# Kernel tuning notes

Measured on AMD Instinct MI355X. Metric: run time of the kernel, lower is better.

## Reference

```python
import jax, jax.numpy as jnp
import numpy as np

B = 32          # graphs per batch
NPG = 512       # nodes per graph
EPG = 2048      # original edges per graph (stored in y[:, -1])
N = B * NPG     # 16384 nodes
E = B * EPG     # 65536 edges
GF = 5          # num_global_features
ETOT = E + N    # edges after add_self_loops

def _lin(k, o, i):
    return jax.random.normal(k, (o, i), jnp.float32) / np.sqrt(i)

def setup_inputs():
    key = jax.random.key(0)
    ks = jax.random.split(key, 20)
    x = jax.random.normal(ks[0], (N,), jnp.float32)
    off = (jnp.arange(B, dtype=jnp.int32) * NPG)[:, None]
    src = (jax.random.randint(ks[1], (B, EPG), 0, NPG, dtype=jnp.int32) + off).reshape(-1)
    dst = (jax.random.randint(ks[2], (B, EPG), 0, NPG, dtype=jnp.int32) + off).reshape(-1)
    edge_index = jnp.stack([src, dst])
    edge_attr = jax.random.normal(ks[3], (E, GF), jnp.float32)
    # last global feature = number of edges per graph (module reads y[:, -1])
    y = jax.random.normal(ks[4], (B, GF), jnp.float32).at[:, -1].set(float(EPG)).reshape(-1)
    batch_vector = jnp.repeat(jnp.arange(B, dtype=jnp.int32), NPG)
    p = dict(
        Wn=_lin(ks[5], 512, 1), bn=jnp.zeros(512, jnp.float32),
        We=_lin(ks[6], 511, GF), be=jnp.zeros(511, jnp.float32),
        Wg=_lin(ks[7], 512, GF), bg=jnp.zeros(512, jnp.float32),
        Wl=_lin(ks[8], 1024, 512), bl=jnp.zeros(1024, jnp.float32),
        Wr=_lin(ks[9], 1024, 512), br=jnp.zeros(1024, jnp.float32),
        Wge=_lin(ks[10], 1024, 511),
        att=jax.random.normal(ks[11], (1024,), jnp.float32) / 32.0,
        bgat=jnp.zeros(1024, jnp.float32),
        Wm=_lin(ks[12], 1024, 1024), bm=jnp.zeros(1024, jnp.float32),
        Wmi=_lin(ks[13], 1024, 1024), bmi=jnp.zeros(1024, jnp.float32),
        Wce=_lin(ks[14], 1024, 512), bce=jnp.zeros(1024, jnp.float32),
        W1=_lin(ks[15], 256, 2048), b1=jnp.zeros(256, jnp.float32),
        W2=_lin(ks[16], 1, 256), b2=jnp.zeros(1, jnp.float32),
    )
    return dict(x=x, edge_index=edge_index, edge_attr=edge_attr, y=y,
                batch_vector=batch_vector, **p)

def _leaky(v, s=0.01):
    return jnp.where(v >= 0, v, s * v)

def _forward(edge_index, batch_vector, x, edge_attr, y, Wn, bn, We, be, Wg, bg,
             Wl, bl, Wr, br, Wge, att, bgat, Wm, bm, Wmi, bmi, Wce, bce,
             W1, b1, W2, b2):
    # add_self_loops (fill_value=1.0 for edge_attr), self loops appended last
    loops = jnp.arange(N, dtype=edge_index.dtype)
    src = jnp.concatenate([edge_index[0], loops])
    dst = jnp.concatenate([edge_index[1], loops])
    ea = jnp.concatenate([edge_attr, jnp.ones((N, GF), edge_attr.dtype)], axis=0)
    # preprocessing MLPs (dropout = identity at inference)
    h = _leaky(x[:, None] @ Wn.T + bn)               # [N, 512]
    e = _leaky(ea @ We.T + be)                       # [ETOT, 511]
    yg = _leaky(y.reshape(B, GF) @ Wg.T + bg)        # [B, 512]
    # GATv2Conv, 1 head, concat, negative_slope=0.2, no self-loop add
    xl = h @ Wl.T + bl                               # source transform [N, 1024]
    xr = h @ Wr.T + br                               # target transform [N, 1024]
    m = _leaky(xl[src] + xr[dst] + e @ Wge.T, 0.2)   # [ETOT, 1024]
    logit = m @ att                                  # [ETOT]
    mx = jax.ops.segment_max(logit, dst, num_segments=N)
    ex = jnp.exp(logit - mx[dst])
    alpha = ex / (jax.ops.segment_sum(ex, dst, num_segments=N)[dst] + 1e-16)
    gat = jax.ops.segment_sum(alpha[:, None] * xl[src], dst, num_segments=N) + bgat
    edge_total = jnp.concatenate([e, alpha[:, None]], axis=1)  # [ETOT, 512]
    # GeneralConv: undirected message, add aggregation, identity skip (in==out)
    hm = gat @ Wm.T + bm
    hmi = gat @ Wmi.T + bmi
    eh = edge_total @ Wce.T + bce                    # [ETOT, 1024]
    deg = jax.ops.segment_sum(jnp.ones((ETOT,), gat.dtype), dst, num_segments=N)
    conv = (jax.ops.segment_sum(hm[src] + eh, dst, num_segments=N)
            + deg[:, None] * hmi + gat)              # [N, 1024]
    # global mean pooling (nodes) and module's contiguous edge batch vector
    nc = jax.ops.segment_sum(jnp.ones((N,), conv.dtype), batch_vector, num_segments=B)
    pn = jax.ops.segment_sum(conv, batch_vector, num_segments=B) / nc[:, None]
    ebatch = jnp.repeat(jnp.arange(B, dtype=jnp.int32), EPG + NPG)
    pe = jax.ops.segment_sum(edge_total, ebatch, num_segments=B) / float(EPG + NPG)
    pooled = jnp.concatenate([pn, pe, yg], axis=1)   # [B, 2048]
    out = _leaky(pooled @ W1.T + b1) @ W2.T + b2
    return jax.nn.sigmoid(out)                       # [B, 1]

def reference(x, edge_index, edge_attr, y, batch_vector, Wn, bn, We, be, Wg, bg,
              Wl, bl, Wr, br, Wge, att, bgat, Wm, bm, Wmi, bmi, Wce, bce,
              W1, b1, W2, b2):
    return _forward(edge_index, batch_vector, x, edge_attr, y, Wn, bn, We, be,
                    Wg, bg, Wl, bl, Wr, br, Wge, att, bgat, Wm, bm, Wmi, bmi,
                    Wce, bce, W1, b1, W2, b2)
```

## Files before the change

kernel.cpp:

```cpp
#include <hip/hip_runtime.h>
#include <cstdint>
#include <cstddef>

#define N_NODES 16384
#define N_EDGES 65536
#define ETOT    81920
#define B_GR    32

typedef __attribute__((ext_vector_type(8))) short bf16x8;
typedef __attribute__((ext_vector_type(4))) float f32x4;

static constexpr size_t OFF_XL    = 0;
static constexpr size_t OFF_XR    = 33554432ULL;
static constexpr size_t OFF_EBF   = 67108864ULL;
static constexpr size_t OFF_SORT  = 67108864ULL;
static constexpr size_t OFF_TAB   = 67125248ULL;
static constexpr size_t TABSZ     = 513ULL*2048ULL*4ULL;
static constexpr size_t OFF_WT    = OFF_TAB + 4*TABSZ;
static constexpr size_t OFF_SEG   = OFF_WT + 4194304ULL;
static constexpr size_t SEGSZ     = 32ULL*2048ULL*4ULL;
static constexpr size_t OFF_ALPHA = 67502336ULL;
static constexpr size_t OFF_ADJ   = 67830016ULL;
static constexpr size_t OFF_WGEP  = 134217728ULL;
static constexpr size_t OFF_LPART = 135266304ULL;
static constexpr size_t OFF_DEG   = 137363456ULL;
static constexpr size_t OFF_ODEG  = 137428992ULL;
static constexpr size_t OFF_CURS  = 137494528ULL;
static constexpr size_t OFF_PG    = 137560064ULL;
static constexpr size_t OFF_PDG   = 137691136ULL;
static constexpr size_t OFF_PGAT  = 137822208ULL;
static constexpr size_t OFF_PS    = 137953280ULL;
static constexpr size_t OFF_PE    = 138018816ULL;
static constexpr size_t OFF_WLOOP = 138084352ULL;
static constexpr size_t OFF_YG    = 138088448ULL;
static constexpr size_t OFF_PN    = 138153984ULL;
static constexpr size_t OFF_OPRE  = 138285056ULL;

__device__ __forceinline__ float leaky01(float v){ return v >= 0.f ? v : 0.01f*v; }
__device__ __forceinline__ float leaky02(float v){ return v >= 0.f ? v : 0.2f*v; }
__device__ __forceinline__ unsigned short f2bf(float f){
  union { float f; unsigned u; } v; v.f = f;
  unsigned r = v.u + 0x7FFFu + ((v.u >> 16) & 1u);
  return (unsigned short)(r >> 16);
}
__device__ __forceinline__ float bf2f(unsigned short h){
  union { unsigned u; float f; } v; v.u = ((unsigned)h) << 16;
  return v.f;
}

__global__ __launch_bounds__(256) void k_prep0(
    const float* __restrict__ Wge, const float* __restrict__ y,
    const float* __restrict__ Wg, const float* __restrict__ bg,
    const float* __restrict__ We, const float* __restrict__ be,
    const float* __restrict__ Wn, const float* __restrict__ bn,
    const float* __restrict__ Wl, const float* __restrict__ Wr,
    float* __restrict__ zone, unsigned short* __restrict__ Wge_p,
    float* __restrict__ yg, float* __restrict__ we_loop,
    float* __restrict__ WT,
    float* __restrict__ sTpos, float* __restrict__ sTneg,
    int* __restrict__ posIdx, int* __restrict__ negIdx, int* __restrict__ meta) {
  __shared__ union {
    float e_lds[512];
    float tile[64][65];
    struct { float tS[512]; int gS[512]; int zflag; } srt;
  } shm;
  int bx = blockIdx.x, tid = threadIdx.x;
  if (bx < 176) {
    ((float4*)zone)[bx*256 + tid] = (float4){0.f,0.f,0.f,0.f};
  } else if (bx < 2224) {
    int gid = (bx-176)*256 + tid;
    int j = gid >> 9, k = gid & 511;
    Wge_p[gid] = (k < 511) ? f2bf(Wge[(size_t)j*511 + k]) : (unsigned short)0;
  } else if (bx < 2288) {
    int gid = (bx-2224)*256 + tid;
    int b = gid >> 9, j = gid & 511;
    float s = bg[j];
    #pragma unroll
    for (int k=0;k<5;k++) s += y[b*5+k]*Wg[j*5+k];
    yg[gid] = leaky01(s);
  } else if (bx < 2292) {
    for (int c = tid; c < 512; c += 256) {
      float v = 0.f;
      if (c < 511) {
        float s = be[c];
        #pragma unroll
        for (int q=0;q<5;q++) s += We[c*5+q];
        v = leaky01(s);
      }
      shm.e_lds[c] = v;
    }
    __syncthreads();
    int j = (bx-2288)*256 + tid;
    float s = 0.f;
    for (int k=0;k<511;k++) s += shm.e_lds[k]*Wge[(size_t)j*511+k];
    we_loop[j] = s;
  } else if (bx < 2548) {
    int t = bx - 2292;
    int jt = t & 31, kt = t >> 5;
    #pragma unroll
    for (int i=0;i<16;i++){
      int idx = tid + i*256;
      int jj = idx >> 6, kk = idx & 63;
      int j = jt*64 + jj, k = kt*64 + kk;
      float v = (j < 1024) ? Wl[(size_t)j*512 + k] : Wr[(size_t)(j-1024)*512 + k];
      shm.tile[kk][jj] = v;
    }
    __syncthreads();
    #pragma unroll
    for (int i=0;i<16;i++){
      int idx = tid + i*256;
      int kk = idx >> 6, jj = idx & 63;
      WT[(size_t)(kt*64 + kk)*2048 + jt*64 + jj] = shm.tile[kk][jj];
    }
  } else {
    const float INF = __builtin_inff();
    if (tid == 0) shm.srt.zflag = 0;
    __syncthreads();
    for (int kk = tid; kk < 512; kk += 256) {
      float wn = Wn[kk], bk = bn[kk];
      int gp; float t;
      if (wn > 0.f)      { gp = 1; t = -bk/wn; }
      else if (wn < 0.f) { gp = 0; t = -bk/wn; }
      else               { gp = 1; t = (bk >= 0.f) ? -INF : INF; }
      shm.srt.tS[kk] = t; shm.srt.gS[kk] = gp;
      if (bk != 0.f) atomicOr(&shm.srt.zflag, 1);
    }
    __syncthreads();
    int cp = 0;
    for (int m = 0; m < 512; m++) cp += shm.srt.gS[m];
    int cn = 512 - cp;
    for (int kk = tid; kk < 512; kk += 256) {
      float t = shm.srt.tS[kk]; int gp = shm.srt.gS[kk];
      int rank = 0;
      for (int m = 0; m < 512; m++) {
        if (shm.srt.gS[m] == gp) {
          float tm = shm.srt.tS[m];
          bool lt = gp ? (tm < t) : (tm > t);
          if (lt || (tm == t && m < kk)) rank++;
        }
      }
      if (gp) { sTpos[rank] = t; posIdx[rank] = kk; }
      else    { sTneg[rank] = t; negIdx[rank] = kk; }
      if (kk >= cp) { sTpos[kk] = INF;  posIdx[kk] = 0; }
      if (kk >= cn) { sTneg[kk] = -INF; negIdx[kk] = 0; }
    }
    if (tid == 0) { meta[0] = cp; meta[1] = cn; meta[2] = (shm.srt.zflag == 0) ? 1 : 0; }
  }
}


__global__ __launch_bounds__(256) void k_tab_sum(
    const float* __restrict__ WT,
    const float* __restrict__ Wn, const float* __restrict__ bn,
    const int* __restrict__ posIdx, const int* __restrict__ negIdx,
    const int* __restrict__ meta,
    float* __restrict__ segAP, float* __restrict__ segAN,
    float* __restrict__ segBP, float* __restrict__ segBN) {
  __shared__ float wnS[512], bnS[512];
  __shared__ int piS[512], niS[512];
  int tid = threadIdx.x;
  for (int i = tid; i < 512; i += 256) {
    wnS[i] = Wn[i]; bnS[i] = bn[i]; piS[i] = posIdx[i]; niS[i] = negIdx[i];
  }
  __syncthreads();
  int seg = blockIdx.x >> 3, jb = blockIdx.x & 7;
  int j = jb*256 + tid;
  int cntP = meta[0], cntN = meta[1], bz = meta[2];
  float aP=0.f, aN=0.f, bP=0.f, bN=0.f;
  for (int i = 0; i < 16; i++) {
    int r = seg*16 + i;
    if (r < cntP) { int k = piS[r]; float w = WT[(size_t)k*2048 + j]; aP += w*wnS[k]; if (!bz) bP += w*bnS[k]; }
    if (r < cntN) { int k = niS[r]; float w = WT[(size_t)k*2048 + j]; aN += w*wnS[k]; if (!bz) bN += w*bnS[k]; }
  }
  segAP[seg*2048 + j] = aP; segAN[seg*2048 + j] = aN;
  if (!bz) { segBP[seg*2048 + j] = bP; segBN[seg*2048 + j] = bN; }
}

__global__ __launch_bounds__(256) void k_tab_write(
    const float* __restrict__ WT,
    const float* __restrict__ Wn, const float* __restrict__ bn,
    const int* __restrict__ posIdx, const int* __restrict__ negIdx,
    const int* __restrict__ meta,
    const float* __restrict__ segAP, const float* __restrict__ segAN,
    const float* __restrict__ segBP, const float* __restrict__ segBN,
    float* __restrict__ SAp, float* __restrict__ SAn,
    float* __restrict__ SBp, float* __restrict__ SBn) {
  __shared__ float wnS[512], bnS[512];
  __shared__ int piS[512], niS[512];
  int tid = threadIdx.x;
  for (int i = tid; i < 512; i += 256) {
    wnS[i] = Wn[i]; bnS[i] = bn[i]; piS[i] = posIdx[i]; niS[i] = negIdx[i];
  }
  __syncthreads();
  int seg = blockIdx.x >> 3, jb = blockIdx.x & 7;
  int j = jb*256 + tid;
  int cntP = meta[0], cntN = meta[1], bz = meta[2];
  float oAP=0.f, oAN=0.f, oBP=0.f, oBN=0.f;
  for (int s = 0; s < seg; s++) {
    oAP += segAP[s*2048 + j]; oAN += segAN[s*2048 + j];
    if (!bz) { oBP += segBP[s*2048 + j]; oBN += segBN[s*2048 + j]; }
  }
  if (seg == 0) {
    SAp[j] = 0.f; SAn[j] = 0.f;
    if (!bz) { SBp[j] = 0.f; SBn[j] = 0.f; }
  }
  for (int i = 0; i < 16; i++) {
    int r = seg*16 + i;
    if (r < cntP) { int k = piS[r]; float w = WT[(size_t)k*2048 + j]; oAP += w*wnS[k]; if (!bz) oBP += w*bnS[k]; }
    if (r < cntN) { int k = niS[r]; float w = WT[(size_t)k*2048 + j]; oAN += w*wnS[k]; if (!bz) oBN += w*bnS[k]; }
    size_t o = (size_t)(r+1)*2048 + j;
    SAp[o] = oAP; SAn[o] = oAN;
    if (!bz) { SBp[o] = oBP; SBn[o] = oBN; }
  }
}

__global__ __launch_bounds__(256) void k_xlxr(
    const float* __restrict__ x,
    const float* __restrict__ sTpos, const float* __restrict__ sTneg,
    const int* __restrict__ meta,
    const float* __restrict__ SAp, const float* __restrict__ SAn,
    const float* __restrict__ SBp, const float* __restrict__ SBn,
    const float* __restrict__ bl, const float* __restrict__ br,
    unsigned short* __restrict__ xl_bf, unsigned short* __restrict__ xr_bf) {
  __shared__ float totA[2048], totB[2048];
  __shared__ float xS[8];
  __shared__ int rpS[8], rnS[8];
  int tid = threadIdx.x, bid = blockIdx.x;
  int cntP = meta[0], cntN = meta[1], bnzero = meta[2];
  for (int i = tid; i < 2048; i += 256) {
    totA[i] = 0.01f*(SAp[(size_t)cntP*2048 + i] + SAn[(size_t)cntN*2048 + i]);
    totB[i] = bnzero ? 0.f : 0.01f*(SBp[(size_t)cntP*2048 + i] + SBn[(size_t)cntN*2048 + i]);
  }
  if (tid < 8) {
    int n = bid*8 + tid;
    float xv = x[n];
    xS[tid] = xv;
    int lo = 0, hi = 512;
    while (lo < hi) { int mid = (lo+hi)>>1; if (sTpos[mid] <= xv) lo = mid+1; else hi = mid; }
    rpS[tid] = lo;
    lo = 0; hi = 512;
    while (lo < hi) { int mid = (lo+hi)>>1; if (sTneg[mid] >= xv) lo = mid+1; else hi = mid; }
    rnS[tid] = lo;
  }
  __syncthreads();
  int j0 = tid*8;
  bool isL = (j0 < 1024);
  const float* bias = isL ? (bl + j0) : (br + (j0 - 1024));
  float4 bb0 = *(const float4*)(bias);
  float4 bb1 = *(const float4*)(bias + 4);
  float bv[8] = {bb0.x,bb0.y,bb0.z,bb0.w,bb1.x,bb1.y,bb1.z,bb1.w};
  unsigned short* O = isL ? xl_bf : xr_bf;
  int jc = j0 & 1023;
  for (int i = 0; i < 8; i++) {
    int n = bid*8 + i;
    float xv = xS[i];
    size_t rp = (size_t)rpS[i]*2048 + j0, rn = (size_t)rnS[i]*2048 + j0;
    float4 a0 = *(const float4*)(SAp + rp); float4 a1 = *(const float4*)(SAp + rp + 4);
    float4 c0 = *(const float4*)(SAn + rn); float4 c1 = *(const float4*)(SAn + rn + 4);
    float pa[8] = {a0.x+c0.x, a0.y+c0.y, a0.z+c0.z, a0.w+c0.w,
                   a1.x+c1.x, a1.y+c1.y, a1.z+c1.z, a1.w+c1.w};
    float pb[8] = {0.f,0.f,0.f,0.f,0.f,0.f,0.f,0.f};
    if (!bnzero) {
      float4 d0 = *(const float4*)(SBp + rp); float4 d1 = *(const float4*)(SBp + rp + 4);
      float4 e0 = *(const float4*)(SBn + rn); float4 e1 = *(const float4*)(SBn + rn + 4);
      pb[0]=d0.x+e0.x; pb[1]=d0.y+e0.y; pb[2]=d0.z+e0.z; pb[3]=d0.w+e0.w;
      pb[4]=d1.x+e1.x; pb[5]=d1.y+e1.y; pb[6]=d1.z+e1.z; pb[7]=d1.w+e1.w;
    }
    unsigned short o[8];
    #pragma unroll
    for (int q=0;q<8;q++) {
      float cA = totA[j0+q] + 0.99f*pa[q];
      float cB = totB[j0+q] + 0.99f*pb[q];
      o[q] = f2bf(xv*cA + cB + bv[q]);
    }
    *(uint4*)(O + (size_t)n*1024 + jc) = *(const uint4*)o;
  }
}

__global__ __launch_bounds__(256) void k_prep_e(
    const float* __restrict__ ea, const float* __restrict__ We, const float* __restrict__ be,
    unsigned short* __restrict__ E_bf,
    const int* __restrict__ ei, int* __restrict__ deg, int* __restrict__ odeg) {
  int blk = blockIdx.x;
  if (blk < 16384) {
    int gid = blk*256 + threadIdx.x;
    int e = gid >> 6, cg = gid & 63;
    int c0 = cg*8;
    const float* e5 = ea + (size_t)e*5;
    float a0=e5[0], a1=e5[1], a2=e5[2], a3=e5[3], a4=e5[4];
    unsigned short o[8];
    #pragma unroll
    for (int j=0;j<8;j++) {
      int c = c0 + j;
      float v = 0.f;
      if (c < 511) {
        const float* w = We + c*5;
        float s = be[c] + a0*w[0] + a1*w[1] + a2*w[2] + a3*w[3] + a4*w[4];
        v = leaky01(s);
      }
      o[j] = f2bf(v);
    }
    ((uint4*)E_bf)[gid] = *(const uint4*)o;
  } else {
    int i = (blk-16384)*256 + threadIdx.x;
    int s, d;
    if (i < N_EDGES) { s = ei[i]; d = ei[N_EDGES + i]; }
    else { s = i - N_EDGES; d = s; }
    atomicAdd(&deg[d], 1);
    atomicAdd(&odeg[s], 1);
  }
}

__global__ void k_fill_adj(const int* __restrict__ ei, int* __restrict__ cursor,
                           int* __restrict__ adj) {
  int i = blockIdx.x*blockDim.x + threadIdx.x;
  int d = (i < N_EDGES) ? ei[N_EDGES + i] : (i - N_EDGES);
  int pos = atomicAdd(&cursor[d], 1);
  if (pos < 64) adj[(size_t)d*64 + pos] = i;
}


__global__ __launch_bounds__(256) void k_mfma_we(
    const unsigned short* __restrict__ E_bf, const unsigned short* __restrict__ Wge_bf,
    const int* __restrict__ ei,
    const unsigned short* __restrict__ xl_bf, const unsigned short* __restrict__ xr_bf,
    const float* __restrict__ att, float* __restrict__ logit_part) {
  __shared__ unsigned short As[2][4096];
  __shared__ unsigned short Bs[2][4096];
  __shared__ float tmp[128];
  int blk = blockIdx.x;
  int xcd = blk & 7, slot = blk >> 3;
  int bx = xcd*64 + (slot >> 3), by = slot & 7;
  int row0 = bx*128, col0 = by*128;
  int tid = threadIdx.x;
  int w = tid >> 6, lane = tid & 63;
  int wm = w >> 1, wn = w & 1;
  int quad = lane >> 4, l16 = lane & 15;
  int ldoff = w*512 + lane*8;
  const unsigned short* gA = E_bf  + (size_t)(row0 + w*16 + l16)*512 + quad*8;
  const unsigned short* gB = Wge_bf + (size_t)(col0 + w*16 + l16)*512 + quad*8;
  f32x4 acc[4][4];
  #pragma unroll
  for (int i=0;i<4;i++)
    #pragma unroll
    for (int j=0;j<4;j++) acc[i][j] = (f32x4){0.f,0.f,0.f,0.f};

  {
    uint4 a0 = *(const uint4*)(gA);
    uint4 a1 = *(const uint4*)(gA + 32768);
    uint4 b0 = *(const uint4*)(gB);
    uint4 b1 = *(const uint4*)(gB + 32768);
    *(uint4*)&As[0][ldoff] = a0; *(uint4*)&As[0][2048+ldoff] = a1;
    *(uint4*)&Bs[0][ldoff] = b0; *(uint4*)&Bs[0][2048+ldoff] = b1;
  }
  __syncthreads();
  int cur = 0;
  #pragma unroll 2
  for (int k0 = 32; k0 <= 512; k0 += 32) {
    uint4 na0, na1, nb0, nb1;
    bool more = (k0 < 512);
    if (more) {
      na0 = *(const uint4*)(gA + k0);
      na1 = *(const uint4*)(gA + 32768 + k0);
      nb0 = *(const uint4*)(gB + k0);
      nb1 = *(const uint4*)(gB + 32768 + k0);
    }
    bf16x8 af[4], bfr[4];
    #pragma unroll
    for (int mi=0;mi<4;mi++)
      af[mi] = *(const bf16x8*)&As[cur][(wm*4+mi)*512 + quad*128 + l16*8];
    #pragma unroll
    for (int ni=0;ni<4;ni++)
      bfr[ni] = *(const bf16x8*)&Bs[cur][(wn*4+ni)*512 + quad*128 + l16*8];
    #pragma unroll
    for (int mi=0;mi<4;mi++)
      #pragma unroll
      for (int ni=0;ni<4;ni++)
        acc[mi][ni] = __builtin_amdgcn_mfma_f32_16x16x32_bf16(af[mi], bfr[ni], acc[mi][ni], 0, 0, 0);
    if (more) {
      *(uint4*)&As[cur^1][ldoff] = na0; *(uint4*)&As[cur^1][2048+ldoff] = na1;
      *(uint4*)&Bs[cur^1][ldoff] = nb0; *(uint4*)&Bs[cur^1][2048+ldoff] = nb1;
    }
    __syncthreads();
    cur ^= 1;
  }
  float att4[4];
  #pragma unroll
  for (int ni=0;ni<4;ni++) att4[ni] = att[col0 + wn*64 + ni*16 + l16];
  float pv[4][4];
  #pragma unroll
  for (int mi=0;mi<4;mi++) {
    #pragma unroll
    for (int r=0;r<4;r++) {
      int e = row0 + wm*64 + mi*16 + quad*4 + r;
      int s = ei[e], d = ei[N_EDGES + e];
      const unsigned short* xlr = xl_bf + (size_t)s*1024;
      const unsigned short* xrr = xr_bf + (size_t)d*1024;
      float p = 0.f;
      #pragma unroll
      for (int ni=0;ni<4;ni++) {
        int col = col0 + wn*64 + ni*16 + l16;
        float z = acc[mi][ni][r] + bf2f(xlr[col]) + bf2f(xrr[col]);
        z = leaky02(z);
        p += z*att4[ni];
      }
      p += __shfl_down(p, 8, 16);
      p += __shfl_down(p, 4, 16);
      p += __shfl_down(p, 2, 16);
      p += __shfl_down(p, 1, 16);
      pv[mi][r] = p;
    }
  }
  if (wn == 1 && l16 == 0) {
    #pragma unroll
    for (int mi=0;mi<4;mi++)
      #pragma unroll
      for (int r=0;r<4;r++)
        tmp[wm*64 + mi*16 + quad*4 + r] = pv[mi][r];
  }
  __syncthreads();
  if (wn == 0 && l16 == 0) {
    #pragma unroll
    for (int mi=0;mi<4;mi++)
      #pragma unroll
      for (int r=0;r<4;r++) {
        int le = wm*64 + mi*16 + quad*4 + r;
        logit_part[(size_t)(row0 + le)*8 + by] = pv[mi][r] + tmp[le];
      }
  }
}

__global__ __launch_bounds__(256) void k_softmax_gat(
    const int* __restrict__ ei, const int* __restrict__ deg, const int* __restrict__ adj,
    const float* __restrict__ logit_part,
    const unsigned short* __restrict__ xl_bf, const unsigned short* __restrict__ xr_bf,
    const float* __restrict__ we_loop, const float* __restrict__ att,
    const float* __restrict__ bgat,
    float* __restrict__ alpha, unsigned short* __restrict__ gat_bf) {
  int blk = blockIdx.x;
  int wid = threadIdx.x >> 6, lane = threadIdx.x & 63;
  int n = ((blk & 7) << 11) + ((blk >> 3) << 2) + wid;
  int c0 = lane*16;

  float sll;
  {
    const uint4* xp = (const uint4*)(xl_bf + (size_t)n*1024 + c0);
    const uint4* rp = (const uint4*)(xr_bf + (size_t)n*1024 + c0);
    uint4 xa0 = xp[0], xa1 = xp[1];
    uint4 xb0 = rp[0], xb1 = rp[1];
    const unsigned short* ua = (const unsigned short*)&xa0;
    const unsigned short* ub = (const unsigned short*)&xb0;
    const unsigned short* ua1 = (const unsigned short*)&xa1;
    const unsigned short* ub1 = (const unsigned short*)&xb1;
    float s = 0.f;
    #pragma unroll
    for (int j=0;j<8;j++) {
      float z = bf2f(ua[j]) + bf2f(ub[j]) + we_loop[c0+j];
      s += leaky02(z) * att[c0+j];
    }
    #pragma unroll
    for (int j=0;j<8;j++) {
      float z = bf2f(ua1[j]) + bf2f(ub1[j]) + we_loop[c0+8+j];
      s += leaky02(z) * att[c0+8+j];
    }
    #pragma unroll
    for (int m=1; m<64; m<<=1) s += __shfl_xor(s, m);
    sll = s;
  }

  int cnt = deg[n];
  if (cnt > 64) cnt = 64;

  float acc[16];
  {
    const float4* bp = (const float4*)(bgat + c0);
    float4 b0 = bp[0], b1 = bp[1], b2 = bp[2], b3 = bp[3];
    acc[0]=b0.x; acc[1]=b0.y; acc[2]=b0.z; acc[3]=b0.w;
    acc[4]=b1.x; acc[5]=b1.y; acc[6]=b1.z; acc[7]=b1.w;
    acc[8]=b2.x; acc[9]=b2.y; acc[10]=b2.z; acc[11]=b2.w;
    acc[12]=b3.x; acc[13]=b3.y; acc[14]=b3.z; acc[15]=b3.w;
  }

  bool act = (lane < cnt);
  int e = 0, src = 0;
  float lg = -1e30f;
  if (act) {
    e = adj[(size_t)n*64 + lane];
    if (e < N_EDGES) {
      const float4* lp = (const float4*)(logit_part + (size_t)e*8);
      float4 q0 = lp[0], q1 = lp[1];
      lg = q0.x+q0.y+q0.z+q0.w+q1.x+q1.y+q1.z+q1.w;
      src = ei[e];
    } else { lg = sll; src = e - N_EDGES; }
  }
  float mx = lg;
  #pragma unroll
  for (int m=1; m<64; m<<=1) mx = fmaxf(mx, __shfl_xor(mx, m));
  float ex = act ? expf(lg - mx) : 0.f;
  float ss = ex;
  #pragma unroll
  for (int m=1; m<64; m<<=1) ss += __shfl_xor(ss, m);
  float a = ex * (1.f/(ss + 1e-16f));
  if (act) alpha[e] = a;
  for (int q = 0; q < cnt; q++) {
    float aq = __shfl(a, q);
    int sq = __shfl(src, q);
    const uint4* xp = (const uint4*)(xl_bf + (size_t)sq*1024 + c0);
    uint4 u0 = xp[0], u1 = xp[1];
    const unsigned short* uu0 = (const unsigned short*)&u0;
    const unsigned short* uu1 = (const unsigned short*)&u1;
    #pragma unroll
    for (int j=0;j<8;j++) acc[j]   += aq * bf2f(uu0[j]);
    #pragma unroll
    for (int j=0;j<8;j++) acc[8+j] += aq * bf2f(uu1[j]);
  }

  unsigned short o[16];
  #pragma unroll
  for (int j=0;j<16;j++) o[j] = f2bf(acc[j]);
  uint4* gp = (uint4*)(gat_bf + (size_t)n*1024 + c0);
  gp[0] = *(const uint4*)&o[0];
  gp[1] = *(const uint4*)&o[8];
}

__global__ __launch_bounds__(256) void k_pool(
    const unsigned short* __restrict__ gat_bf, const int* __restrict__ odeg,
    const int* __restrict__ deg,
    float* __restrict__ P_G, float* __restrict__ P_DG, float* __restrict__ P_gat,
    const float* __restrict__ ea, const float* __restrict__ We, const float* __restrict__ be,
    const float* __restrict__ alpha, float* __restrict__ P_S, float* __restrict__ pe) {
  __shared__ float sea[640];
  __shared__ float sal[128];
  int slot = blockIdx.x, tid = threadIdx.x;
  if (slot < 512) {
    int b = slot >> 4, nc = slot & 15;
    int c4 = tid;
    float a1[4]={0,0,0,0}, a2[4]={0,0,0,0}, a3[4]={0,0,0,0};
    int n0 = b*512 + nc*32;
    for (int i=0;i<32;i++){
      int n = n0 + i;
      ushort4 g4 = ((const ushort4*)(gat_bf + (size_t)n*1024))[c4];
      float od = (float)odeg[n];
      float dg = (float)deg[n];
      float g0 = bf2f(g4.x), g1 = bf2f(g4.y), g2 = bf2f(g4.z), g3 = bf2f(g4.w);
      a1[0]+=od*g0; a1[1]+=od*g1; a1[2]+=od*g2; a1[3]+=od*g3;
      a2[0]+=dg*g0; a2[1]+=dg*g1; a2[2]+=dg*g2; a2[3]+=dg*g3;
      a3[0]+=g0; a3[1]+=g1; a3[2]+=g2; a3[3]+=g3;
    }
    #pragma unroll
    for (int j=0;j<4;j++){
      atomicAdd(&P_G [b*1024 + c4*4+j], a1[j]);
      atomicAdd(&P_DG[b*1024 + c4*4+j], a2[j]);
      atomicAdd(&P_gat[b*1024 + c4*4+j], a3[j]);
    }
  } else {
    int s = slot - 512;
    int b = s & 31, chy = s >> 5;
    int mode = (chy < 20) ? 0 : 1;
    int ch = (chy < 20) ? chy : (chy - 20);
    int c1 = tid, c2 = tid + 256;
    bool v2 = (c2 < 511);
    float w1[5], w2[5]={0,0,0,0,0}, b1v, b2v=0.f;
    #pragma unroll
    for (int q=0;q<5;q++) w1[q] = We[c1*5+q];
    b1v = be[c1];
    if (v2) {
      #pragma unroll
      for (int q=0;q<5;q++) w2[q] = We[c2*5+q];
      b2v = be[c2];
    }
    int base = (mode == 0)
      ? ((ch < 16) ? (b*2048 + ch*128) : (N_EDGES + b*512 + (ch-16)*128))
      : (b*2560 + ch*128);
    for (int i=tid;i<640;i+=256){
      int r = base + i/5;
      sea[i] = (r < N_EDGES) ? ea[(size_t)r*5 + (i%5)] : 1.0f;
    }
    for (int i=tid;i<128;i+=256) sal[i] = alpha[base + i];
    __syncthreads();
    float acc1 = 0.f, acc2 = 0.f;
    for (int rr=0; rr<128; rr++) {
      const float* er = &sea[rr*5];
      acc1 += leaky01(b1v + er[0]*w1[0]+er[1]*w1[1]+er[2]*w1[2]+er[3]*w1[3]+er[4]*w1[4]);
      if (v2) acc2 += leaky01(b2v + er[0]*w2[0]+er[1]*w2[1]+er[2]*w2[2]+er[3]*w2[3]+er[4]*w2[4]);
      else    acc2 += sal[rr];
    }
    if (mode == 0) {
      atomicAdd(&P_S[b*512+c1], acc1);
      atomicAdd(&P_S[b*512+c2], acc2);
    } else {
      const float sc = 1.f/2560.f;
      atomicAdd(&pe[b*512+c1], acc1*sc);
      atomicAdd(&pe[b*512+c2], acc2*sc);
    }
  }
}

__global__ __launch_bounds__(256) void k_pn(
    const float* __restrict__ P_G, const float* __restrict__ P_DG,
    const float* __restrict__ P_S, const float* __restrict__ P_gat,
    const float* __restrict__ Wm, const float* __restrict__ bm,
    const float* __restrict__ Wmi, const float* __restrict__ bmi,
    const float* __restrict__ Wce, const float* __restrict__ bce,
    float* __restrict__ pn, float* __restrict__ out_pre, int* __restrict__ done) {
  __shared__ float sPg[1024], sPdg[1024], sPs[512];
  int blk = blockIdx.x;
  int xcd = blk & 7, slot = blk >> 3;
  int colgrp = xcd*2 + (slot & 1);
  int b = slot >> 1;
  int col0 = colgrp*64;
  int tid = threadIdx.x, w = tid >> 6, lane = tid & 63;
  if (blk == 0 && tid < 32) { out_pre[tid] = 0.f; done[tid] = 0; }
  for (int i=tid;i<1024;i+=256){ sPg[i]=P_G[b*1024+i]; sPdg[i]=P_DG[b*1024+i]; }
  for (int i=tid;i<512;i+=256) sPs[i]=P_S[b*512+i];
  __syncthreads();
  for (int c=0;c<16;c++){
    int j = col0 + w*16 + c;
    const float* wm  = Wm  + (size_t)j*1024;
    const float* wmi = Wmi + (size_t)j*1024;
    const float* wce = Wce + (size_t)j*512;
    float s = 0.f;
    #pragma unroll 4
    for (int i=0;i<16;i++){ int k = lane + i*64; s += sPg[k]*wm[k] + sPdg[k]*wmi[k]; }
    #pragma unroll 4
    for (int i=0;i<8;i++){ int k = lane + i*64; s += sPs[k]*wce[k]; }
    #pragma unroll
    for (int off=32; off; off>>=1) s += __shfl_down(s, off);
    if (lane == 0) {
      pn[b*1024+j] = (s + P_gat[b*1024+j] + 2560.f*(bm[j]+bmi[j]+bce[j])) * (1.f/512.f);
    }
  }
}

__global__ __launch_bounds__(256) void k_final(
    const float* __restrict__ pn, const float* __restrict__ pe, const float* __restrict__ yg,
    const float* __restrict__ W1, const float* __restrict__ b1,
    const float* __restrict__ W2, const float* __restrict__ b2,
    float* __restrict__ out_pre, int* __restrict__ done, float* __restrict__ out) {
  __shared__ float pooled[2048];
  int blk = blockIdx.x;
  int hc = blk & 7, b = blk >> 3;
  int tid = threadIdx.x;
  for (int i=tid;i<1024;i+=256) pooled[i]      = pn[b*1024+i];
  for (int i=tid;i<512;i+=256)  pooled[1024+i] = pe[b*512+i];
  for (int i=tid;i<512;i+=256)  pooled[1536+i] = yg[b*512+i];
  __syncthreads();
  int r = hc*32 + (tid >> 3);
  int seg = tid & 7;
  const float4* w4 = (const float4*)(W1 + (size_t)r*2048 + seg*256);
  const float4* p4 = (const float4*)(pooled + seg*256);
  float s = 0.f;
  #pragma unroll 8
  for (int k=0;k<64;k++){
    float4 w = w4[k]; float4 p = p4[k];
    s += w.x*p.x + w.y*p.y + w.z*p.z + w.w*p.w;
  }
  s += __shfl_down(s, 4, 8);
  s += __shfl_down(s, 2, 8);
  s += __shfl_down(s, 1, 8);
  if (seg == 0) {
    float h = leaky01(s + b1[r]);
    atomicAdd(&out_pre[b], h * W2[r]);
  }
  __syncthreads();
  if (tid == 0) {
    __threadfence();
    if (atomicAdd(&done[b], 1) == 7) {
      float v = atomicAdd(&out_pre[b], 0.f);
      out[b] = 1.f/(1.f + expf(-(v + b2[0])));
    }
  }
}

extern "C" void kernel_launch(void* const* d_in, const int* in_sizes, int n_in,
                              void* d_out, int out_size, void* d_ws, size_t ws_size,
                              hipStream_t stream) {
  const float* x   = (const float*)d_in[0];
  const int*   ei  = (const int*)  d_in[1];
  const float* ea  = (const float*)d_in[2];
  const float* y   = (const float*)d_in[3];
  const float* Wn  = (const float*)d_in[5];
  const float* bn  = (const float*)d_in[6];
  const float* We  = (const float*)d_in[7];
  const float* be  = (const float*)d_in[8];
  const float* Wg  = (const float*)d_in[9];
  const float* bg  = (const float*)d_in[10];
  const float* Wl  = (const float*)d_in[11];
  const float* bl  = (const float*)d_in[12];
  const float* Wr  = (const float*)d_in[13];
  const float* br  = (const float*)d_in[14];
  const float* Wge = (const float*)d_in[15];
  const float* att = (const float*)d_in[16];
  const float* bgat= (const float*)d_in[17];
  const float* Wm  = (const float*)d_in[18];
  const float* bm  = (const float*)d_in[19];
  const float* Wmi = (const float*)d_in[20];
  const float* bmi = (const float*)d_in[21];
  const float* Wce = (const float*)d_in[22];
  const float* bce = (const float*)d_in[23];
  const float* W1  = (const float*)d_in[24];
  const float* b1  = (const float*)d_in[25];
  const float* W2  = (const float*)d_in[26];
  const float* b2  = (const float*)d_in[27];
  float* out = (float*)d_out;

  char* ws = (char*)d_ws;
  unsigned short* xl_bf  = (unsigned short*)(ws + OFF_XL);
  unsigned short* xr_bf  = (unsigned short*)(ws + OFF_XR);
  unsigned short* gat_bf = (unsigned short*)(ws + OFF_XR);
  unsigned short* E_bf   = (unsigned short*)(ws + OFF_EBF);
  unsigned short* Wge_p  = (unsigned short*)(ws + OFF_WGEP);
  float* sTpos  = (float*)(ws + OFF_SORT);
  float* sTneg  = (float*)(ws + OFF_SORT + 2048);
  int*   posIdx = (int*)  (ws + OFF_SORT + 4096);
  int*   negIdx = (int*)  (ws + OFF_SORT + 6144);
  int*   meta   = (int*)  (ws + OFF_SORT + 8192);
  float* SAp    = (float*)(ws + OFF_TAB);
  float* SAn    = (float*)(ws + OFF_TAB + TABSZ);
  float* SBp    = (float*)(ws + OFF_TAB + 2*TABSZ);
  float* SBn    = (float*)(ws + OFF_TAB + 3*TABSZ);
  float* WT     = (float*)(ws + OFF_WT);
  float* segAP  = (float*)(ws + OFF_SEG);
  float* segAN  = (float*)(ws + OFF_SEG + SEGSZ);
  float* segBP  = (float*)(ws + OFF_SEG + 2*SEGSZ);
  float* segBN  = (float*)(ws + OFF_SEG + 3*SEGSZ);
  float* lpart  = (float*)(ws + OFF_LPART);
  int*   done   = (int*)  (ws + OFF_LPART);
  float* zone   = (float*)(ws + OFF_DEG);
  int*   deg    = (int*)  (ws + OFF_DEG);
  int*   odeg   = (int*)  (ws + OFF_ODEG);
  int*   cursor = (int*)  (ws + OFF_CURS);
  float* P_G    = (float*)(ws + OFF_PG);
  float* P_DG   = (float*)(ws + OFF_PDG);
  float* P_gat  = (float*)(ws + OFF_PGAT);
  float* P_S    = (float*)(ws + OFF_PS);
  float* pe     = (float*)(ws + OFF_PE);
  int*   adj    = (int*)  (ws + OFF_ADJ);
  float* alpha  = (float*)(ws + OFF_ALPHA);
  float* we_loop= (float*)(ws + OFF_WLOOP);
  float* yg     = (float*)(ws + OFF_YG);
  float* pn     = (float*)(ws + OFF_PN);
  float* out_pre= (float*)(ws + OFF_OPRE);

  k_prep0<<<dim3(2549), dim3(256), 0, stream>>>(Wge, y, Wg, bg, We, be, Wn, bn, Wl, Wr,
                                                zone, Wge_p, yg, we_loop,
                                                WT, sTpos, sTneg, posIdx, negIdx, meta);
  k_tab_sum<<<dim3(256), dim3(256), 0, stream>>>(WT, Wn, bn, posIdx, negIdx, meta,
                                                 segAP, segAN, segBP, segBN);
  k_tab_write<<<dim3(256), dim3(256), 0, stream>>>(WT, Wn, bn, posIdx, negIdx, meta,
                                                   segAP, segAN, segBP, segBN,
                                                   SAp, SAn, SBp, SBn);
  k_xlxr<<<dim3(2048), dim3(256), 0, stream>>>(x, sTpos, sTneg, meta, SAp, SAn, SBp, SBn,
                                               bl, br, xl_bf, xr_bf);
  k_prep_e<<<dim3(16704), dim3(256), 0, stream>>>(ea, We, be, E_bf, ei, deg, odeg);
  k_mfma_we<<<dim3(4096), dim3(256), 0, stream>>>(E_bf, Wge_p, ei, xl_bf, xr_bf, att, lpart);
  k_fill_adj<<<dim3(320), dim3(256), 0, stream>>>(ei, cursor, adj);
  k_softmax_gat<<<dim3(4096), dim3(256), 0, stream>>>(ei, deg, adj, lpart, xl_bf, xr_bf,
                                                      we_loop, att, bgat, alpha, gat_bf);
  k_pool<<<dim3(1792), dim3(256), 0, stream>>>(gat_bf, odeg, deg, P_G, P_DG, P_gat,
                                               ea, We, be, alpha, P_S, pe);
  k_pn<<<dim3(512), dim3(256), 0, stream>>>(P_G, P_DG, P_S, P_gat, Wm, bm, Wmi, bmi, Wce, bce,
                                            pn, out_pre, done);
  k_final<<<dim3(256), dim3(256), 0, stream>>>(pn, pe, yg, W1, b1, W2, b2, out_pre, done, out);
}
```

Measured before the change: 543.5 us.

## Fuse GAT node pooling into softmax-aggregation kernel, dropping gat_bf round trip

The per-node GAT output is no longer written to global memory as bf16 and re-read by the pooling kernel. Instead, each softmax/aggregation block handles 16 nodes of one graph and accumulates odeg-, deg- and unit-weighted sums into shared memory with atomics. It then flushes them to the per-graph pooled buffers with global atomics. This removes a 32 MB write and read plus the node part of k_pool, at the cost of fewer blocks (1024) and heavy shared-memory atomic traffic.

```diff
diff --git a/kernel.cpp b/kernel.cpp
--- a/kernel.cpp
+++ b/kernel.cpp
@@ -148,7 +148,6 @@
   }
 }
 
-
 __global__ __launch_bounds__(256) void k_tab_sum(
     const float* __restrict__ WT,
     const float* __restrict__ Wn, const float* __restrict__ bn,
@@ -319,7 +318,6 @@
   if (pos < 64) adj[(size_t)d*64 + pos] = i;
 }
 
-
 __global__ __launch_bounds__(256) void k_mfma_we(
     const unsigned short* __restrict__ E_bf, const unsigned short* __restrict__ Wge_bf,
     const int* __restrict__ ei,
@@ -431,168 +429,160 @@
 }
 
 __global__ __launch_bounds__(256) void k_softmax_gat(
-    const int* __restrict__ ei, const int* __restrict__ deg, const int* __restrict__ adj,
+    const int* __restrict__ ei, const int* __restrict__ deg, const int* __restrict__ odeg,
+    const int* __restrict__ adj,
     const float* __restrict__ logit_part,
     const unsigned short* __restrict__ xl_bf, const unsigned short* __restrict__ xr_bf,
     const float* __restrict__ we_loop, const float* __restrict__ att,
     const float* __restrict__ bgat,
-    float* __restrict__ alpha, unsigned short* __restrict__ gat_bf) {
+    float* __restrict__ alpha,
+    float* __restrict__ P_G, float* __restrict__ P_DG, float* __restrict__ P_gat) {
+  __shared__ float sG[1024], sDG[1024], sGat[1024];
   int blk = blockIdx.x;
-  int wid = threadIdx.x >> 6, lane = threadIdx.x & 63;
-  int n = ((blk & 7) << 11) + ((blk >> 3) << 2) + wid;
+  int tid = threadIdx.x;
+  int wid = tid >> 6, lane = tid & 63;
+  int base = ((blk & 7) << 11) + ((blk >> 3) << 4);
+  int b = base >> 9;
   int c0 = lane*16;
 
-  float sll;
-  {
-    const uint4* xp = (const uint4*)(xl_bf + (size_t)n*1024 + c0);
-    const uint4* rp = (const uint4*)(xr_bf + (size_t)n*1024 + c0);
-    uint4 xa0 = xp[0], xa1 = xp[1];
-    uint4 xb0 = rp[0], xb1 = rp[1];
-    const unsigned short* ua = (const unsigned short*)&xa0;
-    const unsigned short* ub = (const unsigned short*)&xb0;
-    const unsigned short* ua1 = (const unsigned short*)&xa1;
-    const unsigned short* ub1 = (const unsigned short*)&xb1;
-    float s = 0.f;
-    #pragma unroll
-    for (int j=0;j<8;j++) {
-      float z = bf2f(ua[j]) + bf2f(ub[j]) + we_loop[c0+j];
-      s += leaky02(z) * att[c0+j];
-    }
-    #pragma unroll
-    for (int j=0;j<8;j++) {
-      float z = bf2f(ua1[j]) + bf2f(ub1[j]) + we_loop[c0+8+j];
-      s += leaky02(z) * att[c0+8+j];
-    }
-    #pragma unroll
-    for (int m=1; m<64; m<<=1) s += __shfl_xor(s, m);
-    sll = s;
-  }
-
-  int cnt = deg[n];
-  if (cnt > 64) cnt = 64;
-
-  float acc[16];
-  {
-    const float4* bp = (const float4*)(bgat + c0);
-    float4 b0 = bp[0], b1 = bp[1], b2 = bp[2], b3 = bp[3];
-    acc[0]=b0.x; acc[1]=b0.y; acc[2]=b0.z; acc[3]=b0.w;
-    acc[4]=b1.x; acc[5]=b1.y; acc[6]=b1.z; acc[7]=b1.w;
-    acc[8]=b2.x; acc[9]=b2.y; acc[10]=b2.z; acc[11]=b2.w;
-    acc[12]=b3.x; acc[13]=b3.y; acc[14]=b3.z; acc[15]=b3.w;
-  }
-
-  bool act = (lane < cnt);
-  int e = 0, src = 0;
-  float lg = -1e30f;
-  if (act) {
-    e = adj[(size_t)n*64 + lane];
-    if (e < N_EDGES) {
-      const float4* lp = (const float4*)(logit_part + (size_t)e*8);
-      float4 q0 = lp[0], q1 = lp[1];
-      lg = q0.x+q0.y+q0.z+q0.w+q1.x+q1.y+q1.z+q1.w;
-      src = ei[e];
-    } else { lg = sll; src = e - N_EDGES; }
-  }
-  float mx = lg;
-  #pragma unroll
-  for (int m=1; m<64; m<<=1) mx = fmaxf(mx, __shfl_xor(mx, m));
-  float ex = act ? expf(lg - mx) : 0.f;
-  float ss = ex;
-  #pragma unroll
-  for (int m=1; m<64; m<<=1) ss += __shfl_xor(ss, m);
-  float a = ex * (1.f/(ss + 1e-16f));
-  if (act) alpha[e] = a;
-  for (int q = 0; q < cnt; q++) {
-    float aq = __shfl(a, q);
-    int sq = __shfl(src, q);
-    const uint4* xp = (const uint4*)(xl_bf + (size_t)sq*1024 + c0);
-    uint4 u0 = xp[0], u1 = xp[1];
-    const unsigned short* uu0 = (const unsigned short*)&u0;
-    const unsigned short* uu1 = (const unsigned short*)&u1;
-    #pragma unroll
-    for (int j=0;j<8;j++) acc[j]   += aq * bf2f(uu0[j]);
-    #pragma unroll
-    for (int j=0;j<8;j++) acc[8+j] += aq * bf2f(uu1[j]);
-  }
-
-  unsigned short o[16];
-  #pragma unroll
-  for (int j=0;j<16;j++) o[j] = f2bf(acc[j]);
-  uint4* gp = (uint4*)(gat_bf + (size_t)n*1024 + c0);
-  gp[0] = *(const uint4*)&o[0];
-  gp[1] = *(const uint4*)&o[8];
+  for (int i = tid; i < 1024; i += 256) { sG[i]=0.f; sDG[i]=0.f; sGat[i]=0.f; }
+  __syncthreads();
+
+  for (int it = 0; it < 4; it++) {
+    int n = base + wid*4 + it;
+
+    float sll;
+    {
+      const uint4* xp = (const uint4*)(xl_bf + (size_t)n*1024 + c0);
+      const uint4* rp = (const uint4*)(xr_bf + (size_t)n*1024 + c0);
+      uint4 xa0 = xp[0], xa1 = xp[1];
+      uint4 xb0 = rp[0], xb1 = rp[1];
+      const unsigned short* ua = (const unsigned short*)&xa0;
+      const unsigned short* ub = (const unsigned short*)&xb0;
+      const unsigned short* ua1 = (const unsigned short*)&xa1;
+      const unsigned short* ub1 = (const unsigned short*)&xb1;
+      float s = 0.f;
+      #pragma unroll
+      for (int j=0;j<8;j++) {
+        float z = bf2f(ua[j]) + bf2f(ub[j]) + we_loop[c0+j];
+        s += leaky02(z) * att[c0+j];
+      }
+      #pragma unroll
+      for (int j=0;j<8;j++) {
+        float z = bf2f(ua1[j]) + bf2f(ub1[j]) + we_loop[c0+8+j];
+        s += leaky02(z) * att[c0+8+j];
+      }
+      #pragma unroll
+      for (int m=1; m<64; m<<=1) s += __shfl_xor(s, m);
+      sll = s;
+    }
+
+    int cnt = deg[n];
+    if (cnt > 64) cnt = 64;
+
+    float acc[16];
+    {
+      const float4* bp = (const float4*)(bgat + c0);
+      float4 b0 = bp[0], b1 = bp[1], b2 = bp[2], b3 = bp[3];
+      acc[0]=b0.x; acc[1]=b0.y; acc[2]=b0.z; acc[3]=b0.w;
+      acc[4]=b1.x; acc[5]=b1.y; acc[6]=b1.z; acc[7]=b1.w;
+      acc[8]=b2.x; acc[9]=b2.y; acc[10]=b2.z; acc[11]=b2.w;
+      acc[12]=b3.x; acc[13]=b3.y; acc[14]=b3.z; acc[15]=b3.w;
+    }
+
+    bool act = (lane < cnt);
+    int e = 0, src = 0;
+    float lg = -1e30f;
+    if (act) {
+      e = adj[(size_t)n*64 + lane];
+      if (e < N_EDGES) {
+        const float4* lp = (const float4*)(logit_part + (size_t)e*8);
+        float4 q0 = lp[0], q1 = lp[1];
+        lg = q0.x+q0.y+q0.z+q0.w+q1.x+q1.y+q1.z+q1.w;
+        src = ei[e];
+      } else { lg = sll; src = e - N_EDGES; }
+    }
+    float mx = lg;
+    #pragma unroll
+    for (int m=1; m<64; m<<=1) mx = fmaxf(mx, __shfl_xor(mx, m));
+    float ex = act ? expf(lg - mx) : 0.f;
+    float ss = ex;
+    #pragma unroll
+    for (int m=1; m<64; m<<=1) ss += __shfl_xor(ss, m);
+    float a = ex * (1.f/(ss + 1e-16f));
+    if (act) alpha[e] = a;
+    for (int q = 0; q < cnt; q++) {
+      float aq = __shfl(a, q);
+      int sq = __shfl(src, q);
+      const uint4* xp = (const uint4*)(xl_bf + (size_t)sq*1024 + c0);
+      uint4 u0 = xp[0], u1 = xp[1];
+      const unsigned short* uu0 = (const unsigned short*)&u0;
+      const unsigned short* uu1 = (const unsigned short*)&u1;
+      #pragma unroll
+      for (int j=0;j<8;j++) acc[j]   += aq * bf2f(uu0[j]);
+      #pragma unroll
+      for (int j=0;j<8;j++) acc[8+j] += aq * bf2f(uu1[j]);
+    }
+
+    float od = (float)odeg[n], dg = (float)deg[n];
+    #pragma unroll
+    for (int j=0;j<16;j++) {
+      atomicAdd(&sG[c0+j],   od*acc[j]);
+      atomicAdd(&sDG[c0+j],  dg*acc[j]);
+      atomicAdd(&sGat[c0+j], acc[j]);
+    }
+  }
+  __syncthreads();
+  for (int i = tid; i < 1024; i += 256) {
+    atomicAdd(&P_G [b*1024+i], sG[i]);
+    atomicAdd(&P_DG[b*1024+i], sDG[i]);
+    atomicAdd(&P_gat[b*1024+i], sGat[i]);
+  }
 }
 
 __global__ __launch_bounds__(256) void k_pool(
-    const unsigned short* __restrict__ gat_bf, const int* __restrict__ odeg,
-    const int* __restrict__ deg,
-    float* __restrict__ P_G, float* __restrict__ P_DG, float* __restrict__ P_gat,
     const float* __restrict__ ea, const float* __restrict__ We, const float* __restrict__ be,
     const float* __restrict__ alpha, float* __restrict__ P_S, float* __restrict__ pe) {
   __shared__ float sea[640];
   __shared__ float sal[128];
-  int slot = blockIdx.x, tid = threadIdx.x;
-  if (slot < 512) {
-    int b = slot >> 4, nc = slot & 15;
-    int c4 = tid;
-    float a1[4]={0,0,0,0}, a2[4]={0,0,0,0}, a3[4]={0,0,0,0};
-    int n0 = b*512 + nc*32;
-    for (int i=0;i<32;i++){
-      int n = n0 + i;
-      ushort4 g4 = ((const ushort4*)(gat_bf + (size_t)n*1024))[c4];
-      float od = (float)odeg[n];
-      float dg = (float)deg[n];
-      float g0 = bf2f(g4.x), g1 = bf2f(g4.y), g2 = bf2f(g4.z), g3 = bf2f(g4.w);
-      a1[0]+=od*g0; a1[1]+=od*g1; a1[2]+=od*g2; a1[3]+=od*g3;
-      a2[0]+=dg*g0; a2[1]+=dg*g1; a2[2]+=dg*g2; a2[3]+=dg*g3;
-      a3[0]+=g0; a3[1]+=g1; a3[2]+=g2; a3[3]+=g3;
-    }
-    #pragma unroll
-    for (int j=0;j<4;j++){
-      atomicAdd(&P_G [b*1024 + c4*4+j], a1[j]);
-      atomicAdd(&P_DG[b*1024 + c4*4+j], a2[j]);
-      atomicAdd(&P_gat[b*1024 + c4*4+j], a3[j]);
-    }
+  int s = blockIdx.x, tid = threadIdx.x;
+  int b = s & 31, chy = s >> 5;
+  int mode = (chy < 20) ? 0 : 1;
+  int ch = (chy < 20) ? chy : (chy - 20);
+  int c1 = tid, c2 = tid + 256;
+  bool v2 = (c2 < 511);
+  float w1[5], w2[5]={0,0,0,0,0}, b1v, b2v=0.f;
+  #pragma unroll
+  for (int q=0;q<5;q++) w1[q] = We[c1*5+q];
+  b1v = be[c1];
+  if (v2) {
+    #pragma unroll
+    for (int q=0;q<5;q++) w2[q] = We[c2*5+q];
+    b2v = be[c2];
+  }
+  int base = (mode == 0)
+    ? ((ch < 16) ? (b*2048 + ch*128) : (N_EDGES + b*512 + (ch-16)*128))
+    : (b*2560 + ch*128);
+  for (int i=tid;i<640;i+=256){
+    int r = base + i/5;
+    sea[i] = (r < N_EDGES) ? ea[(size_t)r*5 + (i%5)] : 1.0f;
+  }
+  for (int i=tid;i<128;i+=256) sal[i] = alpha[base + i];
+  __syncthreads();
+  float acc1 = 0.f, acc2 = 0.f;
+  for (int rr=0; rr<128; rr++) {
+    const float* er = &sea[rr*5];
+    acc1 += leaky01(b1v + er[0]*w1[0]+er[1]*w1[1]+er[2]*w1[2]+er[3]*w1[3]+er[4]*w1[4]);
+    if (v2) acc2 += leaky01(b2v + er[0]*w2[0]+er[1]*w2[1]+er[2]*w2[2]+er[3]*w2[3]+er[4]*w2[4]);
+    else    acc2 += sal[rr];
+  }
+  if (mode == 0) {
+    atomicAdd(&P_S[b*512+c1], acc1);
+    atomicAdd(&P_S[b*512+c2], acc2);
   } else {
-    int s = slot - 512;
-    int b = s & 31, chy = s >> 5;
-    int mode = (chy < 20) ? 0 : 1;
-    int ch = (chy < 20) ? chy : (chy - 20);
-    int c1 = tid, c2 = tid + 256;
-    bool v2 = (c2 < 511);
-    float w1[5], w2[5]={0,0,0,0,0}, b1v, b2v=0.f;
-    #pragma unroll
-    for (int q=0;q<5;q++) w1[q] = We[c1*5+q];
-    b1v = be[c1];
-    if (v2) {
-      #pragma unroll
-      for (int q=0;q<5;q++) w2[q] = We[c2*5+q];
-      b2v = be[c2];
-    }
-    int base = (mode == 0)
-      ? ((ch < 16) ? (b*2048 + ch*128) : (N_EDGES + b*512 + (ch-16)*128))
-      : (b*2560 + ch*128);
-    for (int i=tid;i<640;i+=256){
-      int r = base + i/5;
-      sea[i] = (r < N_EDGES) ? ea[(size_t)r*5 + (i%5)] : 1.0f;
-    }
-    for (int i=tid;i<128;i+=256) sal[i] = alpha[base + i];
-    __syncthreads();
-    float acc1 = 0.f, acc2 = 0.f;
-    for (int rr=0; rr<128; rr++) {
-      const float* er = &sea[rr*5];
-      acc1 += leaky01(b1v + er[0]*w1[0]+er[1]*w1[1]+er[2]*w1[2]+er[3]*w1[3]+er[4]*w1[4]);
-      if (v2) acc2 += leaky01(b2v + er[0]*w2[0]+er[1]*w2[1]+er[2]*w2[2]+er[3]*w2[3]+er[4]*w2[4]);
-      else    acc2 += sal[rr];
-    }
-    if (mode == 0) {
-      atomicAdd(&P_S[b*512+c1], acc1);
-      atomicAdd(&P_S[b*512+c2], acc2);
-    } else {
-      const float sc = 1.f/2560.f;
-      atomicAdd(&pe[b*512+c1], acc1*sc);
-      atomicAdd(&pe[b*512+c2], acc2*sc);
-    }
+    const float sc = 1.f/2560.f;
+    atomicAdd(&pe[b*512+c1], acc1*sc);
+    atomicAdd(&pe[b*512+c2], acc2*sc);
   }
 }
 
@@ -707,7 +697,6 @@
   char* ws = (char*)d_ws;
   unsigned short* xl_bf  = (unsigned short*)(ws + OFF_XL);
   unsigned short* xr_bf  = (unsigned short*)(ws + OFF_XR);
-  unsigned short* gat_bf = (unsigned short*)(ws + OFF_XR);
   unsigned short* E_bf   = (unsigned short*)(ws + OFF_EBF);
   unsigned short* Wge_p  = (unsigned short*)(ws + OFF_WGEP);
   float* sTpos  = (float*)(ws + OFF_SORT);
@@ -755,10 +744,10 @@
   k_prep_e<<<dim3(16704), dim3(256), 0, stream>>>(ea, We, be, E_bf, ei, deg, odeg);
   k_mfma_we<<<dim3(4096), dim3(256), 0, stream>>>(E_bf, Wge_p, ei, xl_bf, xr_bf, att, lpart);
   k_fill_adj<<<dim3(320), dim3(256), 0, stream>>>(ei, cursor, adj);
-  k_softmax_gat<<<dim3(4096), dim3(256), 0, stream>>>(ei, deg, adj, lpart, xl_bf, xr_bf,
-                                                      we_loop, att, bgat, alpha, gat_bf);
-  k_pool<<<dim3(1792), dim3(256), 0, stream>>>(gat_bf, odeg, deg, P_G, P_DG, P_gat,
-                                               ea, We, be, alpha, P_S, pe);
+  k_softmax_gat<<<dim3(1024), dim3(256), 0, stream>>>(ei, deg, odeg, adj, lpart, xl_bf, xr_bf,
+                                                      we_loop, att, bgat, alpha,
+                                                      P_G, P_DG, P_gat);
+  k_pool<<<dim3(1280), dim3(256), 0, stream>>>(ea, We, be, alpha, P_S, pe);
   k_pn<<<dim3(512), dim3(256), 0, stream>>>(P_G, P_DG, P_S, P_gat, Wm, bm, Wmi, bmi, Wce, bce,
                                             pn, out_pre, done);
   k_final<<<dim3(256), dim3(256), 0, stream>>>(pn, pe, yg, W1, b1, W2, b2, out_pre, done, out);
```

New measurement: 785.9 us. 44.6% more time.
